# Kernel optimization log

Measured on AMD Instinct MI355X. Metric: run time of the kernel, lower is better.

## Reference

```python
import math
import jax, jax.numpy as jnp
import numpy as np


def setup_inputs() -> dict:
    key = jax.random.key(0)
    k1, k2 = jax.random.split(key)
    bs, n_heads, ch, T, ratio = 2, 4, 64, 1024, 4
    q = jax.random.normal(k1, (bs, n_heads * ch, T), dtype=jnp.float32)
    kv = jax.random.normal(k2, (bs, n_heads * 2 * ch, T * ratio), dtype=jnp.float32)
    return {"q": q, "kv": kv, "n_heads": n_heads}


def reference(q, kv, n_heads):
    bs, width, length = q.shape
    _, _, length_kv = kv.shape
    ch = width // n_heads
    B = bs * n_heads
    s = int(math.isqrt(length))            # spatial side, length == s*s
    ratio = length_kv // length

    qh = q.reshape(B, ch, s, s).astype(jnp.float32)
    k_, v_ = jnp.split(kv.reshape(B, 2 * ch, length_kv), 2, axis=1)

    # 2-D FFT + fftshift on q and k
    qf = jnp.fft.fftshift(jnp.fft.fftn(qh, axes=(-2, -1)), axes=(-2, -1))
    qf = qf.reshape(B, ch, length)                      # complex64 [B, ch, T]
    kh = k_.reshape(B, ch, ratio, s, s).astype(jnp.float32)
    kf = jnp.fft.fftshift(jnp.fft.fftn(kh, axes=(-2, -1)), axes=(-2, -1))
    kf = kf.reshape(B, ch, length_kv)                   # complex64 [B, ch, T_kv]

    scale = 1.0 / math.sqrt(math.sqrt(ch))
    w = jnp.einsum('bct,bcs->bts', qf * scale, kf * scale)  # complex [B, T, T_kv]

    # softmax over kv axis, applied separately to real and imag parts
    wr = jnp.stack([w.real, w.imag], axis=-1)           # [B, T, T_kv, 2]
    wr = jax.nn.softmax(wr, axis=-2)
    w = jax.lax.complex(wr[..., 0], wr[..., 1])

    # inverse shift + inverse 2-D FFT, keep real part
    w = w.reshape(B, length, ratio, s, s)
    w = jnp.fft.ifftn(jnp.fft.ifftshift(w, axes=(-2, -1)), axes=(-2, -1)).real
    w = w.reshape(B, length, length_kv).astype(kv.dtype)

    a = jnp.einsum('bts,bcs->bct', w, v_)               # [B, ch, T]
    return a.reshape(bs, n_heads * ch, length)
```

## Files before the change

### kernel.cpp

```cpp
#include <hip/hip_runtime.h>
#include <math.h>

typedef _Float16 half8 __attribute__((ext_vector_type(8)));
typedef float f32x16 __attribute__((ext_vector_type(16)));

#define L2E 1.4426950408889634f
#define KPLANE (8*4096*64)
#define QPLANE (8*1024*64)
#define VPLANE (8*64*4096)

__device__ constexpr float FW_R[16] = {
  1.0f, 0.98078528040323044f, 0.92387953251128674f, 0.83146961230254524f,
  0.70710678118654757f, 0.55557023301960218f, 0.38268343236508978f, 0.19509032201612825f,
  0.0f, -0.19509032201612825f, -0.38268343236508978f, -0.55557023301960218f,
  -0.70710678118654757f, -0.83146961230254524f, -0.92387953251128674f, -0.98078528040323044f };
__device__ constexpr float FW_I[16] = {
  -0.0f, -0.19509032201612825f, -0.38268343236508978f, -0.55557023301960218f,
  -0.70710678118654757f, -0.83146961230254524f, -0.92387953251128674f, -0.98078528040323044f,
  -1.0f, -0.98078528040323044f, -0.92387953251128674f, -0.83146961230254524f,
  -0.70710678118654757f, -0.55557023301960218f, -0.38268343236508978f, -0.19509032201612825f };

static __device__ __forceinline__ void fft32(float* xr, float* xi) {
  #pragma unroll
  for (int i = 0; i < 32; i++) {
    int j = ((i & 1) << 4) | ((i & 2) << 2) | (i & 4) | ((i >> 2) & 2) | ((i >> 4) & 1);
    if (j > i) {
      float t = xr[i]; xr[i] = xr[j]; xr[j] = t;
      t = xi[i]; xi[i] = xi[j]; xi[j] = t;
    }
  }
  #pragma unroll
  for (int s = 1; s <= 5; s++) {
    const int len = 1 << s, half = len >> 1;
    #pragma unroll
    for (int j0 = 0; j0 < 32; j0 += len) {
      #pragma unroll
      for (int k = 0; k < half; k++) {
        const float wr = FW_R[k << (5 - s)], wi = FW_I[k << (5 - s)];
        const int a = j0 + k, b = a + half;
        float tr = xr[b] * wr - xi[b] * wi;
        float ti = xr[b] * wi + xi[b] * wr;
        xr[b] = xr[a] - tr; xi[b] = xi[a] - ti;
        xr[a] += tr; xi[a] += ti;
      }
    }
  }
}

__global__ __launch_bounds__(256) void fft2_all(
    const float* __restrict__ q, const float* __restrict__ kv,
    _Float16* __restrict__ KrH, _Float16* __restrict__ KrL,
    _Float16* __restrict__ KiH, _Float16* __restrict__ KiL,
    _Float16* __restrict__ QrH, _Float16* __restrict__ QrL,
    _Float16* __restrict__ QiH, _Float16* __restrict__ QiL,
    _Float16* __restrict__ Vre, _Float16* __restrict__ Vim)
{
  __shared__ float2 G[8 * 1057];
  const int blk = blockIdx.x;
  const int tid = threadIdx.x;
  const int tr = tid >> 5, col = tid & 31;
  int mode, idx;
  if (blk < 64)       { mode = 0; idx = blk; }
  else if (blk < 320) { mode = 1; idx = blk - 64; }
  else                { mode = 2; idx = blk - 320; }
  int co, r, b;
  if (mode == 0) { co = idx & 7; r = 0;              b = idx >> 3; }
  else           { co = idx & 7; r = (idx >> 3) & 3; b = idx >> 5; }
  const int c = co * 8 + tr;
  const float* src;
  int src_off;
  float scale;
  if (mode == 0)      { src = q;  src_off = (b * 64 + c) * 1024;                  scale = 0.35355339059327373f * L2E; }
  else if (mode == 1) { src = kv; src_off = (b * 128 + c) * 4096 + r * 1024;      scale = 0.35355339059327373f; }
  else                { src = kv; src_off = (b * 128 + 64 + c) * 4096 + r * 1024; scale = 1.0f / 1024.0f; }

  float2* Gt = &G[tr * 1057];

  float xr[32], xi[32];
  #pragma unroll
  for (int n1 = 0; n1 < 32; n1++) { xr[n1] = src[src_off + n1 * 32 + col]; xi[n1] = 0.f; }
  fft32(xr, xi);
  #pragma unroll
  for (int u1 = 0; u1 < 32; u1++) Gt[col * 33 + u1] = make_float2(xr[u1], xi[u1]);
  __syncthreads();

  #pragma unroll
  for (int n2 = 0; n2 < 32; n2++) {
    float2 g = Gt[n2 * 33 + col];
    xr[n2] = g.x; xi[n2] = g.y;
  }
  fft32(xr, xi);
  float* yre = xr;
  float* yim = xi;

  const int su1 = (col + 16) & 31;
  if (mode == 2) {
    int o = (b * 64 + c) * 4096 + r * 1024 + su1 * 32;
    half8 hr[4], hi[4];
    #pragma unroll
    for (int g8 = 0; g8 < 4; g8++)
      #pragma unroll
      for (int e = 0; e < 8; e++) {
        int u2 = ((g8 * 8 + e) + 16) & 31;
        hr[g8][e] = (_Float16)(yre[u2] * scale);
        hi[g8][e] = (_Float16)(yim[u2] * scale);
      }
    #pragma unroll
    for (int g8 = 0; g8 < 4; g8++) {
      *(half8*)(Vre + o + g8 * 8) = hr[g8];
      *(half8*)(Vim + o + g8 * 8) = hi[g8];
    }
  } else {
    __syncthreads();
    #pragma unroll
    for (int u2 = 0; u2 < 32; u2++) {
      int su2 = (u2 + 16) & 31;
      Gt[su1 * 33 + su2] = make_float2(yre[u2] * scale, yim[u2] * scale);
    }
    __syncthreads();
    _Float16 *p0, *p1, *p2, *p3;
    int obase;
    if (mode == 0) { p0 = QrH; p1 = QrL; p2 = QiH; p3 = QiL; obase = (b * 1024) * 64 + co * 8; }
    else           { p0 = KrH; p1 = KrL; p2 = KiH; p3 = KiL; obase = (b * 4096 + r * 1024) * 64 + co * 8; }
    #pragma unroll 2
    for (int k = 0; k < 4; k++) {
      int p = tid + k * 256;
      int pl = (p >> 5) * 33 + (p & 31);
      half8 vH, vL, wH, wL;
      #pragma unroll
      for (int t8 = 0; t8 < 8; t8++) {
        float2 yv = G[t8 * 1057 + pl];
        _Float16 rh = (_Float16)yv.x;
        _Float16 ih = (_Float16)yv.y;
        vH[t8] = rh; vL[t8] = (_Float16)(yv.x - (float)rh);
        wH[t8] = ih; wL[t8] = (_Float16)(yv.y - (float)ih);
      }
      int o = obase + p * 64;
      *(half8*)(p0 + o) = vH;
      *(half8*)(p1 + o) = vL;
      *(half8*)(p2 + o) = wH;
      *(half8*)(p3 + o) = wL;
    }
  }
}

static __device__ inline void storeP(unsigned* pb, const float* p, int lh) {
  #pragma unroll
  for (int u = 0; u < 8; u++) {
    int base = ((u & 1) * 2) + ((u >> 1) * 8) + 4 * lh;
    unsigned short h0 = __builtin_bit_cast(unsigned short, (_Float16)p[2 * u]);
    unsigned short h1 = __builtin_bit_cast(unsigned short, (_Float16)p[2 * u + 1]);
    pb[base >> 1] = (unsigned)h0 | ((unsigned)h1 << 16);
  }
}
static __device__ inline half8 loadP(const unsigned* rp) {
  union { uint4 u; half8 h; } U;
  U.u = *(const uint4*)rp;
  return U.h;
}

__global__ __launch_bounds__(512, 1) void attn_mfma(
    const _Float16* __restrict__ KrH, const _Float16* __restrict__ KrL,
    const _Float16* __restrict__ KiH, const _Float16* __restrict__ KiL,
    const _Float16* __restrict__ QrH, const _Float16* __restrict__ QrL,
    const _Float16* __restrict__ QiH, const _Float16* __restrict__ QiL,
    const _Float16* __restrict__ Vre, const _Float16* __restrict__ Vim,
    float* __restrict__ out)
{
  __shared__ __align__(16) _Float16 qlds[4][4][64][8];
  __shared__ __align__(16) unsigned pbufR[8][32][20];
  __shared__ __align__(16) unsigned pbufI[8][32][20];
  __shared__ float mlb[8][32][5];
  __shared__ float obuf[8][32][33];

  const int tid = threadIdx.x;
  const int lane = tid & 63;
  const int warp = tid >> 6;
  const int b = blockIdx.x & 7;
  const int t0 = (blockIdx.x >> 3) << 5;
  const int lm = lane & 31, lh = lane >> 5;

  {
    const _Float16* qp[4] = {QrH, QrL, QiH, QiL};
    #pragma unroll
    for (int jj = 0; jj < 2; jj++) {
      int idx = tid + jj * 512;
      int pl = idx >> 8, ks = (idx >> 6) & 3, ln = idx & 63;
      int t = ln & 31, hh = ln >> 5;
      const _Float16* s = qp[pl] + ((b * 1024 + t0 + t) * 64 + ks * 16 + hh * 8);
      *(half8*)&qlds[pl][ks][ln][0] = *(const half8*)s;
    }
  }
  __syncthreads();

  int kbase = (b * 4096 + warp * 512 + lm) * 64 + lh * 8;
  const int vbase0 = (b * 64 + lm) * 4096 + warp * 512 + lh * 8;
  const int vbase1 = vbase0 + 32 * 4096;

  float m_r = -3e38f, m_i = -3e38f, l_r = 0.f, l_i = 0.f;
  f32x16 Or0 = (f32x16)(0.0f), Or1 = (f32x16)(0.0f);
  f32x16 Oi0 = (f32x16)(0.0f), Oi1 = (f32x16)(0.0f);

  #pragma unroll 1
  for (int it = 0; it < 16; ++it) {
    f32x16 A1 = (f32x16)(0.0f), A2 = (f32x16)(0.0f), SI = (f32x16)(0.0f);
    #pragma unroll
    for (int ks = 0; ks < 4; ks++) {
      half8 qrh = *(const half8*)&qlds[0][ks][lane][0];
      half8 qrl = *(const half8*)&qlds[1][ks][lane][0];
      half8 qih = *(const half8*)&qlds[2][ks][lane][0];
      half8 qil = *(const half8*)&qlds[3][ks][lane][0];
      const int ko = kbase + ks * 16;
      half8 krh = *(const half8*)(KrH + ko);
      half8 krl = *(const half8*)(KrL + ko);
      half8 kih = *(const half8*)(KiH + ko);
      half8 kil = *(const half8*)(KiL + ko);
      A1 = __builtin_amdgcn_mfma_f32_32x32x16_f16(krh, qrh, A1, 0, 0, 0);
      A2 = __builtin_amdgcn_mfma_f32_32x32x16_f16(kih, qih, A2, 0, 0, 0);
      SI = __builtin_amdgcn_mfma_f32_32x32x16_f16(kih, qrh, SI, 0, 0, 0);
      A1 = __builtin_amdgcn_mfma_f32_32x32x16_f16(krh, qrl, A1, 0, 0, 0);
      A2 = __builtin_amdgcn_mfma_f32_32x32x16_f16(kih, qil, A2, 0, 0, 0);
      SI = __builtin_amdgcn_mfma_f32_32x32x16_f16(krh, qih, SI, 0, 0, 0);
      A1 = __builtin_amdgcn_mfma_f32_32x32x16_f16(krl, qrh, A1, 0, 0, 0);
      A2 = __builtin_amdgcn_mfma_f32_32x32x16_f16(kil, qih, A2, 0, 0, 0);
      SI = __builtin_amdgcn_mfma_f32_32x32x16_f16(kil, qrh, SI, 0, 0, 0);
      SI = __builtin_amdgcn_mfma_f32_32x32x16_f16(kih, qrl, SI, 0, 0, 0);
      SI = __builtin_amdgcn_mfma_f32_32x32x16_f16(krl, qih, SI, 0, 0, 0);
      SI = __builtin_amdgcn_mfma_f32_32x32x16_f16(krh, qil, SI, 0, 0, 0);
    }

    float sre[16], sim[16];
    #pragma unroll
    for (int rr = 0; rr < 16; rr++) { sre[rr] = A1[rr] - A2[rr]; sim[rr] = SI[rr]; }

    float mtr = sre[0], mti = sim[0];
    #pragma unroll
    for (int rr = 1; rr < 16; rr++) { mtr = fmaxf(mtr, sre[rr]); mti = fmaxf(mti, sim[rr]); }
    mtr = fmaxf(mtr, __shfl_xor(mtr, 32));
    mti = fmaxf(mti, __shfl_xor(mti, 32));

    float pr[16], pi[16];
    {
      float mn = fmaxf(m_r, mtr);
      if (__ballot(mtr > m_r + 11.5f)) {
        float al = exp2f(m_r - mn);
        l_r *= al; m_r = mn;
        #pragma unroll
        for (int rr = 0; rr < 16; rr++) { Or0[rr] *= al; Or1[rr] *= al; }
      }
      float sm = 0.f;
      #pragma unroll
      for (int rr = 0; rr < 16; rr++) { pr[rr] = exp2f(sre[rr] - m_r); sm += pr[rr]; }
      l_r += sm + __shfl_xor(sm, 32);
    }
    {
      float mn = fmaxf(m_i, mti);
      if (__ballot(mti > m_i + 11.5f)) {
        float al = exp2f(m_i - mn);
        l_i *= al; m_i = mn;
        #pragma unroll
        for (int rr = 0; rr < 16; rr++) { Oi0[rr] *= al; Oi1[rr] *= al; }
      }
      float sm = 0.f;
      #pragma unroll
      for (int rr = 0; rr < 16; rr++) { pi[rr] = exp2f(sim[rr] - m_i); sm += pi[rr]; }
      l_i += sm + __shfl_xor(sm, 32);
    }

    storeP(&pbufR[warp][lm][0], pr, lh);
    storeP(&pbufI[warp][lm][0], pi, lh);

    #pragma unroll
    for (int h = 0; h < 2; h++) {
      half8 pfr = loadP(&pbufR[warp][lm][h * 8 + 4 * lh]);
      half8 pfi = loadP(&pbufI[warp][lm][h * 8 + 4 * lh]);
      const int vo = it * 32 + h * 16;
      half8 v0r = *(const half8*)(Vre + vbase0 + vo);
      half8 v0i = *(const half8*)(Vim + vbase0 + vo);
      half8 v1r = *(const half8*)(Vre + vbase1 + vo);
      half8 v1i = *(const half8*)(Vim + vbase1 + vo);
      Or0 = __builtin_amdgcn_mfma_f32_32x32x16_f16(v0r, pfr, Or0, 0, 0, 0);
      Oi0 = __builtin_amdgcn_mfma_f32_32x32x16_f16(v0i, pfi, Oi0, 0, 0, 0);
      Or1 = __builtin_amdgcn_mfma_f32_32x32x16_f16(v1r, pfr, Or1, 0, 0, 0);
      Oi1 = __builtin_amdgcn_mfma_f32_32x32x16_f16(v1i, pfi, Oi1, 0, 0, 0);
    }
    kbase += 32 * 64;
  }

  if (lane < 32) {
    mlb[warp][lane][0] = m_r; mlb[warp][lane][1] = l_r;
    mlb[warp][lane][2] = m_i; mlb[warp][lane][3] = l_i;
  }
  __syncthreads();
  float Mr = -3e38f, Mi = -3e38f;
  #pragma unroll
  for (int w = 0; w < 8; w++) {
    Mr = fmaxf(Mr, mlb[w][lm][0]);
    Mi = fmaxf(Mi, mlb[w][lm][2]);
  }
  float Lr = 0.f, Li = 0.f;
  #pragma unroll
  for (int w = 0; w < 8; w++) {
    Lr += mlb[w][lm][1] * exp2f(mlb[w][lm][0] - Mr);
    Li += mlb[w][lm][3] * exp2f(mlb[w][lm][2] - Mi);
  }
  const float fr = exp2f(m_r - Mr) / Lr;
  const float fi = exp2f(m_i - Mi) / Li;

  #pragma unroll
  for (int rr = 0; rr < 16; rr++) {
    int cl = (rr & 3) + 8 * (rr >> 2) + 4 * lh;
    obuf[warp][cl][lm] = Or0[rr] * fr + Oi0[rr] * fi;
  }
  __syncthreads();
  {
    int c = tid >> 4, t2 = (tid & 15) * 2;
    float2 acc = make_float2(0.f, 0.f);
    #pragma unroll
    for (int w = 0; w < 8; w++) { acc.x += obuf[w][c][t2]; acc.y += obuf[w][c][t2 + 1]; }
    *(float2*)&out[(b * 64 + c) * 1024 + t0 + t2] = acc;
  }
  __syncthreads();
  #pragma unroll
  for (int rr = 0; rr < 16; rr++) {
    int cl = (rr & 3) + 8 * (rr >> 2) + 4 * lh;
    obuf[warp][cl][lm] = Or1[rr] * fr + Oi1[rr] * fi;
  }
  __syncthreads();
  {
    int c = tid >> 4, t2 = (tid & 15) * 2;
    float2 acc = make_float2(0.f, 0.f);
    #pragma unroll
    for (int w = 0; w < 8; w++) { acc.x += obuf[w][c][t2]; acc.y += obuf[w][c][t2 + 1]; }
    *(float2*)&out[(b * 64 + 32 + c) * 1024 + t0 + t2] = acc;
  }
}

extern "C" void kernel_launch(void* const* d_in, const int* in_sizes, int n_in,
                              void* d_out, int out_size, void* d_ws, size_t ws_size,
                              hipStream_t stream) {
  const float* q  = (const float*)d_in[0];
  const float* kv = (const float*)d_in[1];
  _Float16* base = (_Float16*)d_ws;
  _Float16* KrH = base;
  _Float16* KrL = KrH + KPLANE;
  _Float16* KiH = KrL + KPLANE;
  _Float16* KiL = KiH + KPLANE;
  _Float16* QrH = KiL + KPLANE;
  _Float16* QrL = QrH + QPLANE;
  _Float16* QiH = QrL + QPLANE;
  _Float16* QiL = QiH + QPLANE;
  _Float16* Vre = QiL + QPLANE;
  _Float16* Vim = Vre + VPLANE;
  float* out = (float*)d_out;

  fft2_all<<<576, 256, 0, stream>>>(q, kv, KrH, KrL, KiH, KiL,
                                    QrH, QrL, QiH, QiL, Vre, Vim);
  attn_mfma<<<256, 512, 0, stream>>>(KrH, KrL, KiH, KiL,
                                     QrH, QrL, QiH, QiL, Vre, Vim, out);
}
```

Measured before the change: 121.6 us.

## Prefetch next K tile into registers and fold real-part subtraction into MFMA

K fragments for the next iteration are now loaded into a double-buffered register set while the softmax and PV MFMAs of the current tile run, so global-load latency is hidden. The real part is accumulated directly into a single accumulator by storing negated Qi copies in shared memory, which removes the separate A2 accumulator and the subtraction. s_setprio is raised around MFMA sections. The costs are more registers (32 half8 of K), extra LDS, and a prefetch at the final iteration that reads past the warp's K slice and may go out of bounds for the last batch.

```diff
diff --git a/kernel.cpp b/kernel.cpp
--- a/kernel.cpp
+++ b/kernel.cpp
@@ -167,7 +167,7 @@
     const _Float16* __restrict__ Vre, const _Float16* __restrict__ Vim,
     float* __restrict__ out)
 {
-  __shared__ __align__(16) _Float16 qlds[4][4][64][8];
+  __shared__ __align__(16) _Float16 qlds[6][4][64][8];
   __shared__ __align__(16) unsigned pbufR[8][32][20];
   __shared__ __align__(16) unsigned pbufI[8][32][20];
   __shared__ float mlb[8][32][5];
@@ -181,19 +181,20 @@
   const int lm = lane & 31, lh = lane >> 5;
 
   {
-    const _Float16* qp[4] = {QrH, QrL, QiH, QiL};
-    #pragma unroll
-    for (int jj = 0; jj < 2; jj++) {
+    const _Float16* qp[6] = {QrH, QrL, QiH, QiL, QiH, QiL};
+    #pragma unroll
+    for (int jj = 0; jj < 3; jj++) {
       int idx = tid + jj * 512;
       int pl = idx >> 8, ks = (idx >> 6) & 3, ln = idx & 63;
       int t = ln & 31, hh = ln >> 5;
-      const _Float16* s = qp[pl] + ((b * 1024 + t0 + t) * 64 + ks * 16 + hh * 8);
-      *(half8*)&qlds[pl][ks][ln][0] = *(const half8*)s;
-    }
-  }
-  __syncthreads();
-
-  int kbase = (b * 4096 + warp * 512 + lm) * 64 + lh * 8;
+      half8 v = *(const half8*)(qp[pl] + ((b * 1024 + t0 + t) * 64 + ks * 16 + hh * 8));
+      if (pl >= 4) v = -v;
+      *(half8*)&qlds[pl][ks][ln][0] = v;
+    }
+  }
+  __syncthreads();
+
+  const int kbase0 = (b * 4096 + warp * 512 + lm) * 64 + lh * 8;
   const int vbase0 = (b * 64 + lm) * 4096 + warp * 512 + lh * 8;
   const int vbase1 = vbase0 + 32 * 4096;
 
@@ -201,41 +202,59 @@
   f32x16 Or0 = (f32x16)(0.0f), Or1 = (f32x16)(0.0f);
   f32x16 Oi0 = (f32x16)(0.0f), Oi1 = (f32x16)(0.0f);
 
-  #pragma unroll 1
-  for (int it = 0; it < 16; ++it) {
-    f32x16 A1 = (f32x16)(0.0f), A2 = (f32x16)(0.0f), SI = (f32x16)(0.0f);
+  half8 kA[16], kB[16];
+  #pragma unroll
+  for (int ks = 0; ks < 4; ks++) {
+    kA[ks * 4 + 0] = *(const half8*)(KrH + kbase0 + ks * 16);
+    kA[ks * 4 + 1] = *(const half8*)(KrL + kbase0 + ks * 16);
+    kA[ks * 4 + 2] = *(const half8*)(KiH + kbase0 + ks * 16);
+    kA[ks * 4 + 3] = *(const half8*)(KiL + kbase0 + ks * 16);
+  }
+
+  auto iter = [&](int it, half8 (&kC)[16], half8 (&kN)[16]) {
+    f32x16 A1 = (f32x16)(0.0f), SI = (f32x16)(0.0f);
+    __builtin_amdgcn_s_setprio(1);
     #pragma unroll
     for (int ks = 0; ks < 4; ks++) {
       half8 qrh = *(const half8*)&qlds[0][ks][lane][0];
       half8 qrl = *(const half8*)&qlds[1][ks][lane][0];
       half8 qih = *(const half8*)&qlds[2][ks][lane][0];
       half8 qil = *(const half8*)&qlds[3][ks][lane][0];
-      const int ko = kbase + ks * 16;
-      half8 krh = *(const half8*)(KrH + ko);
-      half8 krl = *(const half8*)(KrL + ko);
-      half8 kih = *(const half8*)(KiH + ko);
-      half8 kil = *(const half8*)(KiL + ko);
+      half8 qnh = *(const half8*)&qlds[4][ks][lane][0];
+      half8 qnl = *(const half8*)&qlds[5][ks][lane][0];
+      half8 krh = kC[ks * 4 + 0];
+      half8 krl = kC[ks * 4 + 1];
+      half8 kih = kC[ks * 4 + 2];
+      half8 kil = kC[ks * 4 + 3];
       A1 = __builtin_amdgcn_mfma_f32_32x32x16_f16(krh, qrh, A1, 0, 0, 0);
-      A2 = __builtin_amdgcn_mfma_f32_32x32x16_f16(kih, qih, A2, 0, 0, 0);
+      A1 = __builtin_amdgcn_mfma_f32_32x32x16_f16(kih, qnh, A1, 0, 0, 0);
       SI = __builtin_amdgcn_mfma_f32_32x32x16_f16(kih, qrh, SI, 0, 0, 0);
       A1 = __builtin_amdgcn_mfma_f32_32x32x16_f16(krh, qrl, A1, 0, 0, 0);
-      A2 = __builtin_amdgcn_mfma_f32_32x32x16_f16(kih, qil, A2, 0, 0, 0);
+      A1 = __builtin_amdgcn_mfma_f32_32x32x16_f16(kih, qnl, A1, 0, 0, 0);
       SI = __builtin_amdgcn_mfma_f32_32x32x16_f16(krh, qih, SI, 0, 0, 0);
       A1 = __builtin_amdgcn_mfma_f32_32x32x16_f16(krl, qrh, A1, 0, 0, 0);
-      A2 = __builtin_amdgcn_mfma_f32_32x32x16_f16(kil, qih, A2, 0, 0, 0);
+      A1 = __builtin_amdgcn_mfma_f32_32x32x16_f16(kil, qnh, A1, 0, 0, 0);
       SI = __builtin_amdgcn_mfma_f32_32x32x16_f16(kil, qrh, SI, 0, 0, 0);
       SI = __builtin_amdgcn_mfma_f32_32x32x16_f16(kih, qrl, SI, 0, 0, 0);
       SI = __builtin_amdgcn_mfma_f32_32x32x16_f16(krl, qih, SI, 0, 0, 0);
       SI = __builtin_amdgcn_mfma_f32_32x32x16_f16(krh, qil, SI, 0, 0, 0);
     }
-
-    float sre[16], sim[16];
-    #pragma unroll
-    for (int rr = 0; rr < 16; rr++) { sre[rr] = A1[rr] - A2[rr]; sim[rr] = SI[rr]; }
-
-    float mtr = sre[0], mti = sim[0];
-    #pragma unroll
-    for (int rr = 1; rr < 16; rr++) { mtr = fmaxf(mtr, sre[rr]); mti = fmaxf(mti, sim[rr]); }
+    __builtin_amdgcn_s_setprio(0);
+
+    {
+      const int kn = kbase0 + (it + 1) * 32 * 64;
+      #pragma unroll
+      for (int ks = 0; ks < 4; ks++) {
+        kN[ks * 4 + 0] = *(const half8*)(KrH + kn + ks * 16);
+        kN[ks * 4 + 1] = *(const half8*)(KrL + kn + ks * 16);
+        kN[ks * 4 + 2] = *(const half8*)(KiH + kn + ks * 16);
+        kN[ks * 4 + 3] = *(const half8*)(KiL + kn + ks * 16);
+      }
+    }
+
+    float mtr = A1[0], mti = SI[0];
+    #pragma unroll
+    for (int rr = 1; rr < 16; rr++) { mtr = fmaxf(mtr, A1[rr]); mti = fmaxf(mti, SI[rr]); }
     mtr = fmaxf(mtr, __shfl_xor(mtr, 32));
     mti = fmaxf(mti, __shfl_xor(mti, 32));
 
@@ -250,7 +269,7 @@
       }
       float sm = 0.f;
       #pragma unroll
-      for (int rr = 0; rr < 16; rr++) { pr[rr] = exp2f(sre[rr] - m_r); sm += pr[rr]; }
+      for (int rr = 0; rr < 16; rr++) { pr[rr] = exp2f(A1[rr] - m_r); sm += pr[rr]; }
       l_r += sm + __shfl_xor(sm, 32);
     }
     {
@@ -263,13 +282,14 @@
       }
       float sm = 0.f;
       #pragma unroll
-      for (int rr = 0; rr < 16; rr++) { pi[rr] = exp2f(sim[rr] - m_i); sm += pi[rr]; }
+      for (int rr = 0; rr < 16; rr++) { pi[rr] = exp2f(SI[rr] - m_i); sm += pi[rr]; }
       l_i += sm + __shfl_xor(sm, 32);
     }
 
     storeP(&pbufR[warp][lm][0], pr, lh);
     storeP(&pbufI[warp][lm][0], pi, lh);
 
+    __builtin_amdgcn_s_setprio(1);
     #pragma unroll
     for (int h = 0; h < 2; h++) {
       half8 pfr = loadP(&pbufR[warp][lm][h * 8 + 4 * lh]);
@@ -284,7 +304,13 @@
       Or1 = __builtin_amdgcn_mfma_f32_32x32x16_f16(v1r, pfr, Or1, 0, 0, 0);
       Oi1 = __builtin_amdgcn_mfma_f32_32x32x16_f16(v1i, pfi, Oi1, 0, 0, 0);
     }
-    kbase += 32 * 64;
+    __builtin_amdgcn_s_setprio(0);
+  };
+
+  #pragma unroll 1
+  for (int it2 = 0; it2 < 8; ++it2) {
+    iter(2 * it2, kA, kB);
+    iter(2 * it2 + 1, kB, kA);
   }
 
   if (lane < 32) {
```

Result: slower. 183.4 us (+50.8%).

## Prefetch half of next K tile into LDS via global_load_lds during softmax

Applied to the files above, without the earlier changes.

Adds asynchronous global-to-LDS loads for the first two k-slices of the next iteration's K planes. They are issued right after the QK MFMAs, so the loads overlap with the softmax and PV work. The LDS staging buffer is unioned with the output reduction buffer so shared memory use stays bounded. The other half of K is still loaded directly from global. The per-iteration vmcnt(0) wait also stalls on the V loads, and the LDS reads use a plain per-warp buffer with no swizzle, so bank conflicts or wait serialization could offset the gain.

```diff
diff --git a/kernel.cpp b/kernel.cpp
--- a/kernel.cpp
+++ b/kernel.cpp
@@ -159,6 +159,12 @@
   return U.h;
 }
 
+static __device__ __forceinline__ void gload_lds16(const _Float16* g, _Float16* l) {
+  __builtin_amdgcn_global_load_lds(
+      (const __attribute__((address_space(1))) void*)g,
+      (__attribute__((address_space(3))) void*)l, 16, 0, 0);
+}
+
 __global__ __launch_bounds__(512, 1) void attn_mfma(
     const _Float16* __restrict__ KrH, const _Float16* __restrict__ KrL,
     const _Float16* __restrict__ KiH, const _Float16* __restrict__ KiL,
@@ -171,7 +177,11 @@
   __shared__ __align__(16) unsigned pbufR[8][32][20];
   __shared__ __align__(16) unsigned pbufI[8][32][20];
   __shared__ float mlb[8][32][5];
-  __shared__ float obuf[8][32][33];
+  union KO {
+    _Float16 kst[8][4][2][512];
+    float obuf[8][32][33];
+  };
+  __shared__ __align__(16) KO u;
 
   const int tid = threadIdx.x;
   const int lane = tid & 63;
@@ -191,11 +201,21 @@
       *(half8*)&qlds[pl][ks][ln][0] = *(const half8*)s;
     }
   }
-  __syncthreads();
-
-  int kbase = (b * 4096 + warp * 512 + lm) * 64 + lh * 8;
+
+  const int kbase0 = (b * 4096 + warp * 512 + lm) * 64 + lh * 8;
   const int vbase0 = (b * 64 + lm) * 4096 + warp * 512 + lh * 8;
   const int vbase1 = vbase0 + 32 * 4096;
+
+  {
+    #pragma unroll
+    for (int ks2 = 0; ks2 < 2; ks2++) {
+      gload_lds16(KrH + kbase0 + ks2 * 16, &u.kst[warp][0][ks2][0]);
+      gload_lds16(KrL + kbase0 + ks2 * 16, &u.kst[warp][1][ks2][0]);
+      gload_lds16(KiH + kbase0 + ks2 * 16, &u.kst[warp][2][ks2][0]);
+      gload_lds16(KiL + kbase0 + ks2 * 16, &u.kst[warp][3][ks2][0]);
+    }
+  }
+  __syncthreads();
 
   float m_r = -3e38f, m_i = -3e38f, l_r = 0.f, l_i = 0.f;
   f32x16 Or0 = (f32x16)(0.0f), Or1 = (f32x16)(0.0f);
@@ -203,6 +223,9 @@
 
   #pragma unroll 1
   for (int it = 0; it < 16; ++it) {
+    const int kbase = kbase0 + it * 32 * 64;
+    asm volatile("s_waitcnt vmcnt(0)" ::: "memory");
+
     f32x16 A1 = (f32x16)(0.0f), A2 = (f32x16)(0.0f), SI = (f32x16)(0.0f);
     #pragma unroll
     for (int ks = 0; ks < 4; ks++) {
@@ -210,11 +233,19 @@
       half8 qrl = *(const half8*)&qlds[1][ks][lane][0];
       half8 qih = *(const half8*)&qlds[2][ks][lane][0];
       half8 qil = *(const half8*)&qlds[3][ks][lane][0];
-      const int ko = kbase + ks * 16;
-      half8 krh = *(const half8*)(KrH + ko);
-      half8 krl = *(const half8*)(KrL + ko);
-      half8 kih = *(const half8*)(KiH + ko);
-      half8 kil = *(const half8*)(KiL + ko);
+      half8 krh, krl, kih, kil;
+      if (ks < 2) {
+        krh = *(const half8*)&u.kst[warp][0][ks][lane * 8];
+        krl = *(const half8*)&u.kst[warp][1][ks][lane * 8];
+        kih = *(const half8*)&u.kst[warp][2][ks][lane * 8];
+        kil = *(const half8*)&u.kst[warp][3][ks][lane * 8];
+      } else {
+        const int ko = kbase + ks * 16;
+        krh = *(const half8*)(KrH + ko);
+        krl = *(const half8*)(KrL + ko);
+        kih = *(const half8*)(KiH + ko);
+        kil = *(const half8*)(KiL + ko);
+      }
       A1 = __builtin_amdgcn_mfma_f32_32x32x16_f16(krh, qrh, A1, 0, 0, 0);
       A2 = __builtin_amdgcn_mfma_f32_32x32x16_f16(kih, qih, A2, 0, 0, 0);
       SI = __builtin_amdgcn_mfma_f32_32x32x16_f16(kih, qrh, SI, 0, 0, 0);
@@ -229,6 +260,18 @@
       SI = __builtin_amdgcn_mfma_f32_32x32x16_f16(krh, qil, SI, 0, 0, 0);
     }
 
+    __builtin_amdgcn_sched_barrier(0);
+    if (it < 15) {
+      const int kn = kbase0 + (it + 1) * 32 * 64;
+      #pragma unroll
+      for (int ks2 = 0; ks2 < 2; ks2++) {
+        gload_lds16(KrH + kn + ks2 * 16, &u.kst[warp][0][ks2][0]);
+        gload_lds16(KrL + kn + ks2 * 16, &u.kst[warp][1][ks2][0]);
+        gload_lds16(KiH + kn + ks2 * 16, &u.kst[warp][2][ks2][0]);
+        gload_lds16(KiL + kn + ks2 * 16, &u.kst[warp][3][ks2][0]);
+      }
+    }
+
     float sre[16], sim[16];
     #pragma unroll
     for (int rr = 0; rr < 16; rr++) { sre[rr] = A1[rr] - A2[rr]; sim[rr] = SI[rr]; }
@@ -284,7 +327,6 @@
       Or1 = __builtin_amdgcn_mfma_f32_32x32x16_f16(v1r, pfr, Or1, 0, 0, 0);
       Oi1 = __builtin_amdgcn_mfma_f32_32x32x16_f16(v1i, pfi, Oi1, 0, 0, 0);
     }
-    kbase += 32 * 64;
   }
 
   if (lane < 32) {
@@ -310,28 +352,28 @@
   #pragma unroll
   for (int rr = 0; rr < 16; rr++) {
     int cl = (rr & 3) + 8 * (rr >> 2) + 4 * lh;
-    obuf[warp][cl][lm] = Or0[rr] * fr + Oi0[rr] * fi;
+    u.obuf[warp][cl][lm] = Or0[rr] * fr + Oi0[rr] * fi;
   }
   __syncthreads();
   {
     int c = tid >> 4, t2 = (tid & 15) * 2;
     float2 acc = make_float2(0.f, 0.f);
     #pragma unroll
-    for (int w = 0; w < 8; w++) { acc.x += obuf[w][c][t2]; acc.y += obuf[w][c][t2 + 1]; }
+    for (int w = 0; w < 8; w++) { acc.x += u.obuf[w][c][t2]; acc.y += u.obuf[w][c][t2 + 1]; }
     *(float2*)&out[(b * 64 + c) * 1024 + t0 + t2] = acc;
   }
   __syncthreads();
   #pragma unroll
   for (int rr = 0; rr < 16; rr++) {
     int cl = (rr & 3) + 8 * (rr >> 2) + 4 * lh;
-    obuf[warp][cl][lm] = Or1[rr] * fr + Oi1[rr] * fi;
+    u.obuf[warp][cl][lm] = Or1[rr] * fr + Oi1[rr] * fi;
   }
   __syncthreads();
   {
     int c = tid >> 4, t2 = (tid & 15) * 2;
     float2 acc = make_float2(0.f, 0.f);
     #pragma unroll
-    for (int w = 0; w < 8; w++) { acc.x += obuf[w][c][t2]; acc.y += obuf[w][c][t2 + 1]; }
+    for (int w = 0; w < 8; w++) { acc.x += u.obuf[w][c][t2]; acc.y += u.obuf[w][c][t2 + 1]; }
     *(float2*)&out[(b * 64 + 32 + c) * 1024 + t0 + t2] = acc;
   }
 }
```

New measurement: 124.0 us. 1.02x slower.

## Switch attention kernel to 16x16 MFMA tiles with 16 queries per block

Applied to the files above, without the earlier changes.

The attention kernel now uses 16x16x32 MFMA instructions with 16 query rows per block instead of 32, which doubles the grid to 512 blocks. Launch bounds are raised so up to four blocks can share a CU. Negated copies of the imaginary Q planes are staged in LDS so the real-part products fold into one accumulator, dropping the separate A2 accumulator and its subtraction. The aim is lower register pressure and better latency hiding through occupancy. In exchange, K and V are re-read from global memory by twice as many blocks, and the epilogue needs more barriers.

```diff
diff --git a/kernel.cpp b/kernel.cpp
--- a/kernel.cpp
+++ b/kernel.cpp
@@ -2,7 +2,7 @@
 #include <math.h>
 
 typedef _Float16 half8 __attribute__((ext_vector_type(8)));
-typedef float f32x16 __attribute__((ext_vector_type(16)));
+typedef float f32x4 __attribute__((ext_vector_type(4)));
 
 #define L2E 1.4426950408889634f
 #define KPLANE (8*4096*64)
@@ -144,22 +144,20 @@
   }
 }
 
-static __device__ inline void storeP(unsigned* pb, const float* p, int lh) {
-  #pragma unroll
-  for (int u = 0; u < 8; u++) {
-    int base = ((u & 1) * 2) + ((u >> 1) * 8) + 4 * lh;
-    unsigned short h0 = __builtin_bit_cast(unsigned short, (_Float16)p[2 * u]);
-    unsigned short h1 = __builtin_bit_cast(unsigned short, (_Float16)p[2 * u + 1]);
-    pb[base >> 1] = (unsigned)h0 | ((unsigned)h1 << 16);
-  }
-}
-static __device__ inline half8 loadP(const unsigned* rp) {
+static __device__ inline unsigned packh2(float a, float b) {
+  unsigned short h0 = __builtin_bit_cast(unsigned short, (_Float16)a);
+  unsigned short h1 = __builtin_bit_cast(unsigned short, (_Float16)b);
+  return (unsigned)h0 | ((unsigned)h1 << 16);
+}
+static __device__ inline half8 loadP16(const unsigned* rp) {
   union { uint4 u; half8 h; } U;
   U.u = *(const uint4*)rp;
   return U.h;
 }
 
-__global__ __launch_bounds__(512, 1) void attn_mfma(
+#define MFMA16(A, B, C) __builtin_amdgcn_mfma_f32_16x16x32_f16(A, B, C, 0, 0, 0)
+
+__global__ __launch_bounds__(512, 4) void attn_mfma(
     const _Float16* __restrict__ KrH, const _Float16* __restrict__ KrL,
     const _Float16* __restrict__ KiH, const _Float16* __restrict__ KiL,
     const _Float16* __restrict__ QrH, const _Float16* __restrict__ QrL,
@@ -167,127 +165,169 @@
     const _Float16* __restrict__ Vre, const _Float16* __restrict__ Vim,
     float* __restrict__ out)
 {
-  __shared__ __align__(16) _Float16 qlds[4][4][64][8];
-  __shared__ __align__(16) unsigned pbufR[8][32][20];
-  __shared__ __align__(16) unsigned pbufI[8][32][20];
-  __shared__ float mlb[8][32][5];
-  __shared__ float obuf[8][32][33];
+  __shared__ __align__(16) _Float16 qlds[6][2][64][8];
+  __shared__ __align__(16) unsigned pbufR[8][16][20];
+  __shared__ __align__(16) unsigned pbufI[8][16][20];
+  __shared__ float mlb[8][16][4];
+  __shared__ float obuf[8][16][17];
 
   const int tid = threadIdx.x;
   const int lane = tid & 63;
   const int warp = tid >> 6;
   const int b = blockIdx.x & 7;
-  const int t0 = (blockIdx.x >> 3) << 5;
-  const int lm = lane & 31, lh = lane >> 5;
+  const int t0 = (blockIdx.x >> 3) << 4;
+  const int t = lane & 15, grp = lane >> 4;
 
   {
-    const _Float16* qp[4] = {QrH, QrL, QiH, QiL};
+    const _Float16* qp[6] = {QrH, QrL, QiH, QiL, QiH, QiL};
     #pragma unroll
     for (int jj = 0; jj < 2; jj++) {
       int idx = tid + jj * 512;
-      int pl = idx >> 8, ks = (idx >> 6) & 3, ln = idx & 63;
-      int t = ln & 31, hh = ln >> 5;
-      const _Float16* s = qp[pl] + ((b * 1024 + t0 + t) * 64 + ks * 16 + hh * 8);
-      *(half8*)&qlds[pl][ks][ln][0] = *(const half8*)s;
+      if (idx < 768) {
+        int pl = idx >> 7, ks = (idx >> 6) & 1, l = idx & 63;
+        half8 v = *(const half8*)(qp[pl] +
+            ((b * 1024 + t0 + (l & 15)) * 64 + ks * 32 + (l >> 4) * 8));
+        if (pl >= 4) v = -v;
+        *(half8*)&qlds[pl][ks][l][0] = v;
+      }
     }
   }
   __syncthreads();
 
-  int kbase = (b * 4096 + warp * 512 + lm) * 64 + lh * 8;
-  const int vbase0 = (b * 64 + lm) * 4096 + warp * 512 + lh * 8;
-  const int vbase1 = vbase0 + 32 * 4096;
-
+  const int sbase = warp * 512;
   float m_r = -3e38f, m_i = -3e38f, l_r = 0.f, l_i = 0.f;
-  f32x16 Or0 = (f32x16)(0.0f), Or1 = (f32x16)(0.0f);
-  f32x16 Oi0 = (f32x16)(0.0f), Oi1 = (f32x16)(0.0f);
+  f32x4 OrA = (f32x4)(0.f), OrB = (f32x4)(0.f), OrC = (f32x4)(0.f), OrD = (f32x4)(0.f);
+  f32x4 OiA = (f32x4)(0.f), OiB = (f32x4)(0.f), OiC = (f32x4)(0.f), OiD = (f32x4)(0.f);
 
   #pragma unroll 1
   for (int it = 0; it < 16; ++it) {
-    f32x16 A1 = (f32x16)(0.0f), A2 = (f32x16)(0.0f), SI = (f32x16)(0.0f);
-    #pragma unroll
-    for (int ks = 0; ks < 4; ks++) {
+    const int s0 = sbase + it * 32;
+    const int ka0 = (b * 4096 + s0 + t) * 64 + grp * 8;
+    const int ka1 = ka0 + 16 * 64;
+
+    f32x4 A1a = (f32x4)(0.f), SIa = (f32x4)(0.f);
+    f32x4 A1b = (f32x4)(0.f), SIb = (f32x4)(0.f);
+    #pragma unroll
+    for (int ks = 0; ks < 2; ks++) {
       half8 qrh = *(const half8*)&qlds[0][ks][lane][0];
       half8 qrl = *(const half8*)&qlds[1][ks][lane][0];
       half8 qih = *(const half8*)&qlds[2][ks][lane][0];
       half8 qil = *(const half8*)&qlds[3][ks][lane][0];
-      const int ko = kbase + ks * 16;
-      half8 krh = *(const half8*)(KrH + ko);
-      half8 krl = *(const half8*)(KrL + ko);
-      half8 kih = *(const half8*)(KiH + ko);
-      half8 kil = *(const half8*)(KiL + ko);
-      A1 = __builtin_amdgcn_mfma_f32_32x32x16_f16(krh, qrh, A1, 0, 0, 0);
-      A2 = __builtin_amdgcn_mfma_f32_32x32x16_f16(kih, qih, A2, 0, 0, 0);
-      SI = __builtin_amdgcn_mfma_f32_32x32x16_f16(kih, qrh, SI, 0, 0, 0);
-      A1 = __builtin_amdgcn_mfma_f32_32x32x16_f16(krh, qrl, A1, 0, 0, 0);
-      A2 = __builtin_amdgcn_mfma_f32_32x32x16_f16(kih, qil, A2, 0, 0, 0);
-      SI = __builtin_amdgcn_mfma_f32_32x32x16_f16(krh, qih, SI, 0, 0, 0);
-      A1 = __builtin_amdgcn_mfma_f32_32x32x16_f16(krl, qrh, A1, 0, 0, 0);
-      A2 = __builtin_amdgcn_mfma_f32_32x32x16_f16(kil, qih, A2, 0, 0, 0);
-      SI = __builtin_amdgcn_mfma_f32_32x32x16_f16(kil, qrh, SI, 0, 0, 0);
-      SI = __builtin_amdgcn_mfma_f32_32x32x16_f16(kih, qrl, SI, 0, 0, 0);
-      SI = __builtin_amdgcn_mfma_f32_32x32x16_f16(krl, qih, SI, 0, 0, 0);
-      SI = __builtin_amdgcn_mfma_f32_32x32x16_f16(krh, qil, SI, 0, 0, 0);
-    }
-
-    float sre[16], sim[16];
-    #pragma unroll
-    for (int rr = 0; rr < 16; rr++) { sre[rr] = A1[rr] - A2[rr]; sim[rr] = SI[rr]; }
-
-    float mtr = sre[0], mti = sim[0];
-    #pragma unroll
-    for (int rr = 1; rr < 16; rr++) { mtr = fmaxf(mtr, sre[rr]); mti = fmaxf(mti, sim[rr]); }
+      half8 qnh = *(const half8*)&qlds[4][ks][lane][0];
+      half8 qnl = *(const half8*)&qlds[5][ks][lane][0];
+      {
+        const int ko = ka0 + ks * 32;
+        half8 krh = *(const half8*)(KrH + ko);
+        half8 krl = *(const half8*)(KrL + ko);
+        half8 kih = *(const half8*)(KiH + ko);
+        half8 kil = *(const half8*)(KiL + ko);
+        A1a = MFMA16(krh, qrh, A1a);
+        A1a = MFMA16(kih, qnh, A1a);
+        SIa = MFMA16(kih, qrh, SIa);
+        A1a = MFMA16(krh, qrl, A1a);
+        A1a = MFMA16(kih, qnl, A1a);
+        SIa = MFMA16(krh, qih, SIa);
+        A1a = MFMA16(krl, qrh, A1a);
+        A1a = MFMA16(kil, qnh, A1a);
+        SIa = MFMA16(kil, qrh, SIa);
+        SIa = MFMA16(kih, qrl, SIa);
+        SIa = MFMA16(krl, qih, SIa);
+        SIa = MFMA16(krh, qil, SIa);
+      }
+      {
+        const int ko = ka1 + ks * 32;
+        half8 krh = *(const half8*)(KrH + ko);
+        half8 krl = *(const half8*)(KrL + ko);
+        half8 kih = *(const half8*)(KiH + ko);
+        half8 kil = *(const half8*)(KiL + ko);
+        A1b = MFMA16(krh, qrh, A1b);
+        A1b = MFMA16(kih, qnh, A1b);
+        SIb = MFMA16(kih, qrh, SIb);
+        A1b = MFMA16(krh, qrl, A1b);
+        A1b = MFMA16(kih, qnl, A1b);
+        SIb = MFMA16(krh, qih, SIb);
+        A1b = MFMA16(krl, qrh, A1b);
+        A1b = MFMA16(kil, qnh, A1b);
+        SIb = MFMA16(kil, qrh, SIb);
+        SIb = MFMA16(kih, qrl, SIb);
+        SIb = MFMA16(krl, qih, SIb);
+        SIb = MFMA16(krh, qil, SIb);
+      }
+    }
+
+    float mtr = fmaxf(fmaxf(fmaxf(A1a[0], A1a[1]), fmaxf(A1a[2], A1a[3])),
+                      fmaxf(fmaxf(A1b[0], A1b[1]), fmaxf(A1b[2], A1b[3])));
+    float mti = fmaxf(fmaxf(fmaxf(SIa[0], SIa[1]), fmaxf(SIa[2], SIa[3])),
+                      fmaxf(fmaxf(SIb[0], SIb[1]), fmaxf(SIb[2], SIb[3])));
+    mtr = fmaxf(mtr, __shfl_xor(mtr, 16));
     mtr = fmaxf(mtr, __shfl_xor(mtr, 32));
+    mti = fmaxf(mti, __shfl_xor(mti, 16));
     mti = fmaxf(mti, __shfl_xor(mti, 32));
 
-    float pr[16], pi[16];
+    float pr[8], pi[8];
     {
       float mn = fmaxf(m_r, mtr);
       if (__ballot(mtr > m_r + 11.5f)) {
         float al = exp2f(m_r - mn);
         l_r *= al; m_r = mn;
-        #pragma unroll
-        for (int rr = 0; rr < 16; rr++) { Or0[rr] *= al; Or1[rr] *= al; }
+        OrA *= al; OrB *= al; OrC *= al; OrD *= al;
       }
       float sm = 0.f;
       #pragma unroll
-      for (int rr = 0; rr < 16; rr++) { pr[rr] = exp2f(sre[rr] - m_r); sm += pr[rr]; }
-      l_r += sm + __shfl_xor(sm, 32);
+      for (int r = 0; r < 4; r++) { pr[r] = exp2f(A1a[r] - m_r); sm += pr[r]; }
+      #pragma unroll
+      for (int r = 0; r < 4; r++) { pr[4 + r] = exp2f(A1b[r] - m_r); sm += pr[4 + r]; }
+      sm += __shfl_xor(sm, 16);
+      sm += __shfl_xor(sm, 32);
+      l_r += sm;
     }
     {
       float mn = fmaxf(m_i, mti);
       if (__ballot(mti > m_i + 11.5f)) {
         float al = exp2f(m_i - mn);
         l_i *= al; m_i = mn;
-        #pragma unroll
-        for (int rr = 0; rr < 16; rr++) { Oi0[rr] *= al; Oi1[rr] *= al; }
+        OiA *= al; OiB *= al; OiC *= al; OiD *= al;
       }
       float sm = 0.f;
       #pragma unroll
-      for (int rr = 0; rr < 16; rr++) { pi[rr] = exp2f(sim[rr] - m_i); sm += pi[rr]; }
-      l_i += sm + __shfl_xor(sm, 32);
-    }
-
-    storeP(&pbufR[warp][lm][0], pr, lh);
-    storeP(&pbufI[warp][lm][0], pi, lh);
-
-    #pragma unroll
-    for (int h = 0; h < 2; h++) {
-      half8 pfr = loadP(&pbufR[warp][lm][h * 8 + 4 * lh]);
-      half8 pfi = loadP(&pbufI[warp][lm][h * 8 + 4 * lh]);
-      const int vo = it * 32 + h * 16;
-      half8 v0r = *(const half8*)(Vre + vbase0 + vo);
-      half8 v0i = *(const half8*)(Vim + vbase0 + vo);
-      half8 v1r = *(const half8*)(Vre + vbase1 + vo);
-      half8 v1i = *(const half8*)(Vim + vbase1 + vo);
-      Or0 = __builtin_amdgcn_mfma_f32_32x32x16_f16(v0r, pfr, Or0, 0, 0, 0);
-      Oi0 = __builtin_amdgcn_mfma_f32_32x32x16_f16(v0i, pfi, Oi0, 0, 0, 0);
-      Or1 = __builtin_amdgcn_mfma_f32_32x32x16_f16(v1r, pfr, Or1, 0, 0, 0);
-      Oi1 = __builtin_amdgcn_mfma_f32_32x32x16_f16(v1i, pfi, Oi1, 0, 0, 0);
-    }
-    kbase += 32 * 64;
-  }
-
-  if (lane < 32) {
+      for (int r = 0; r < 4; r++) { pi[r] = exp2f(SIa[r] - m_i); sm += pi[r]; }
+      #pragma unroll
+      for (int r = 0; r < 4; r++) { pi[4 + r] = exp2f(SIb[r] - m_i); sm += pi[4 + r]; }
+      sm += __shfl_xor(sm, 16);
+      sm += __shfl_xor(sm, 32);
+      l_i += sm;
+    }
+
+    {
+      unsigned* pbR = &pbufR[warp][t][0];
+      unsigned* pbI = &pbufI[warp][t][0];
+      #pragma unroll
+      for (int st = 0; st < 2; st++) {
+        int base = st * 8 + grp * 2;
+        pbR[base]     = packh2(pr[st * 4 + 0], pr[st * 4 + 1]);
+        pbR[base + 1] = packh2(pr[st * 4 + 2], pr[st * 4 + 3]);
+        pbI[base]     = packh2(pi[st * 4 + 0], pi[st * 4 + 1]);
+        pbI[base + 1] = packh2(pi[st * 4 + 2], pi[st * 4 + 3]);
+      }
+    }
+
+    {
+      half8 pfr = loadP16(&pbufR[warp][t][grp * 4]);
+      half8 pfi = loadP16(&pbufI[warp][t][grp * 4]);
+      const int va = (b * 64 + t) * 4096 + s0 + grp * 8;
+      half8 v;
+      v = *(const half8*)(Vre + va);               OrA = MFMA16(v, pfr, OrA);
+      v = *(const half8*)(Vim + va);               OiA = MFMA16(v, pfi, OiA);
+      v = *(const half8*)(Vre + va + 16 * 4096);   OrB = MFMA16(v, pfr, OrB);
+      v = *(const half8*)(Vim + va + 16 * 4096);   OiB = MFMA16(v, pfi, OiB);
+      v = *(const half8*)(Vre + va + 32 * 4096);   OrC = MFMA16(v, pfr, OrC);
+      v = *(const half8*)(Vim + va + 32 * 4096);   OiC = MFMA16(v, pfi, OiC);
+      v = *(const half8*)(Vre + va + 48 * 4096);   OrD = MFMA16(v, pfr, OrD);
+      v = *(const half8*)(Vim + va + 48 * 4096);   OiD = MFMA16(v, pfi, OiD);
+    }
+  }
+
+  if (lane < 16) {
     mlb[warp][lane][0] = m_r; mlb[warp][lane][1] = l_r;
     mlb[warp][lane][2] = m_i; mlb[warp][lane][3] = l_i;
   }
@@ -295,44 +335,34 @@
   float Mr = -3e38f, Mi = -3e38f;
   #pragma unroll
   for (int w = 0; w < 8; w++) {
-    Mr = fmaxf(Mr, mlb[w][lm][0]);
-    Mi = fmaxf(Mi, mlb[w][lm][2]);
+    Mr = fmaxf(Mr, mlb[w][t][0]);
+    Mi = fmaxf(Mi, mlb[w][t][2]);
   }
   float Lr = 0.f, Li = 0.f;
   #pragma unroll
   for (int w = 0; w < 8; w++) {
-    Lr += mlb[w][lm][1] * exp2f(mlb[w][lm][0] - Mr);
-    Li += mlb[w][lm][3] * exp2f(mlb[w][lm][2] - Mi);
+    Lr += mlb[w][t][1] * exp2f(mlb[w][t][0] - Mr);
+    Li += mlb[w][t][3] * exp2f(mlb[w][t][2] - Mi);
   }
   const float fr = exp2f(m_r - Mr) / Lr;
   const float fi = exp2f(m_i - Mi) / Li;
 
-  #pragma unroll
-  for (int rr = 0; rr < 16; rr++) {
-    int cl = (rr & 3) + 8 * (rr >> 2) + 4 * lh;
-    obuf[warp][cl][lm] = Or0[rr] * fr + Oi0[rr] * fi;
-  }
-  __syncthreads();
-  {
-    int c = tid >> 4, t2 = (tid & 15) * 2;
-    float2 acc = make_float2(0.f, 0.f);
-    #pragma unroll
-    for (int w = 0; w < 8; w++) { acc.x += obuf[w][c][t2]; acc.y += obuf[w][c][t2 + 1]; }
-    *(float2*)&out[(b * 64 + c) * 1024 + t0 + t2] = acc;
-  }
-  __syncthreads();
-  #pragma unroll
-  for (int rr = 0; rr < 16; rr++) {
-    int cl = (rr & 3) + 8 * (rr >> 2) + 4 * lh;
-    obuf[warp][cl][lm] = Or1[rr] * fr + Oi1[rr] * fi;
-  }
-  __syncthreads();
-  {
-    int c = tid >> 4, t2 = (tid & 15) * 2;
-    float2 acc = make_float2(0.f, 0.f);
-    #pragma unroll
-    for (int w = 0; w < 8; w++) { acc.x += obuf[w][c][t2]; acc.y += obuf[w][c][t2 + 1]; }
-    *(float2*)&out[(b * 64 + 32 + c) * 1024 + t0 + t2] = acc;
+  #pragma unroll 1
+  for (int q4 = 0; q4 < 4; q4++) {
+    f32x4 oR = (q4 == 0) ? OrA : (q4 == 1) ? OrB : (q4 == 2) ? OrC : OrD;
+    f32x4 oI = (q4 == 0) ? OiA : (q4 == 1) ? OiB : (q4 == 2) ? OiC : OiD;
+    __syncthreads();
+    #pragma unroll
+    for (int r = 0; r < 4; r++)
+      obuf[warp][grp * 4 + r][t] = oR[r] * fr + oI[r] * fi;
+    __syncthreads();
+    if (tid < 256) {
+      int c = tid >> 4, tt = tid & 15;
+      float acc = 0.f;
+      #pragma unroll
+      for (int w = 0; w < 8; w++) acc += obuf[w][c][tt];
+      out[(b * 64 + q4 * 16 + c) * 1024 + t0 + tt] = acc;
+    }
   }
 }
 
@@ -356,6 +386,6 @@
 
   fft2_all<<<576, 256, 0, stream>>>(q, kv, KrH, KrL, KiH, KiL,
                                     QrH, QrL, QiH, QiL, Vre, Vim);
-  attn_mfma<<<256, 512, 0, stream>>>(KrH, KrL, KiH, KiL,
+  attn_mfma<<<512, 512, 0, stream>>>(KrH, KrL, KiH, KiL,
                                      QrH, QrL, QiH, QiL, Vre, Vim, out);
 }
```

Result: slower. 244.0 us (+100.7%).
